# Kernel optimization log

Measured on AMD Instinct MI355X. Metric: run time of the kernel, lower is better.

Reference implementation:

```python
import jax, jax.numpy as jnp
import numpy as np

B, N, F_IN, F_OUT = 8, 2048, 128, 64
ALPHA = 0.2  # LeakyReLU negative slope
NEG_INF = -9e15


def setup_inputs() -> dict:
    key = jax.random.key(0)
    k1, k2, k3, k4 = jax.random.split(key, 4)
    h = jax.random.normal(k1, (B, N, F_IN), dtype=jnp.float32)
    adj = jax.random.randint(k2, (B, N, N), 0, 2, dtype=jnp.int32)
    # xavier_uniform with gain=1.414 approximated by scaled normals (values are arbitrary params)
    W = jax.random.normal(k3, (F_IN, F_OUT), dtype=jnp.float32) * (1.414 * np.sqrt(2.0 / (F_IN + F_OUT)))
    a = jax.random.normal(k4, (2 * F_OUT, 1), dtype=jnp.float32) * (1.414 * np.sqrt(2.0 / (2 * F_OUT + 1)))
    return {"h": h, "adj": adj, "W": W, "a": a}


def reference(h, adj, W, a):
    # Wh: [B, N, F_out]
    Wh = jnp.einsum('bnf,fo->bno', h, W)
    Fo = W.shape[1]
    a1 = a[:Fo, 0]   # [F_out]
    a2 = a[Fo:, 0]   # [F_out]
    # e[b,i,j] = leakyrelu(Wh[b,i]@a1 + Wh[b,j]@a2)  (== cat(Wh_i,Wh_j)@a, same math, no N^2*2F blowup)
    e1 = jnp.einsum('bno,o->bn', Wh, a1)  # [B, N]
    e2 = jnp.einsum('bno,o->bn', Wh, a2)  # [B, N]
    e = e1[:, :, None] + e2[:, None, :]   # [B, N, N]
    e = jnp.where(e > 0, e, ALPHA * e)    # LeakyReLU
    e = jnp.where(adj > 0, e, NEG_INF)    # mask non-edges
    attention = jax.nn.softmax(e, axis=-1)
    # dropout is identity in inference mode (deterministic reference)
    h_prime = jnp.einsum('bij,bjo->bio', attention, Wh)  # [B, N, F_out]
    return jax.nn.elu(h_prime)  # concat=True branch
```

## Files before the change

kernel.cpp:

```cpp
#include <hip/hip_runtime.h>
#include <hip/hip_bf16.h>

#define BB 8
#define NN 2048
#define FIN 128
#define FO 64
#define ALPHA 0.2f
#define SPLITS 4

typedef __attribute__((ext_vector_type(8))) short bf16x8;
typedef __attribute__((ext_vector_type(4))) float f32x4;
typedef __attribute__((ext_vector_type(4))) int i32x4;

__device__ inline short f2bf(float x) {
    unsigned u = __float_as_uint(x);
    u += 0x7fffu + ((u >> 16) & 1u);
    return (short)(u >> 16);
}

__global__ __launch_bounds__(256) void wh_kernel(
    const float* __restrict__ h, const float* __restrict__ W,
    const float* __restrict__ a, float* __restrict__ e1, float* __restrict__ e2,
    __hip_bfloat16* __restrict__ whT)
{
    __shared__ float hs[32][FIN];
    const int r0 = blockIdx.x * 32;
    const int t = threadIdx.x;
    const float4* hsrc = (const float4*)(h + (size_t)r0 * FIN);
    float4* hdst = (float4*)(&hs[0][0]);
#pragma unroll
    for (int k = 0; k < 4; k++) hdst[t + 256 * k] = hsrc[t + 256 * k];
    __syncthreads();

    const int o = t & 63;
    const int wv = t >> 6;
    float acc[8];
#pragma unroll
    for (int rr = 0; rr < 8; rr++) acc[rr] = 0.f;

    for (int f = 0; f < FIN; f += 4) {
        const float w0 = W[(f + 0) * FO + o];
        const float w1 = W[(f + 1) * FO + o];
        const float w2 = W[(f + 2) * FO + o];
        const float w3 = W[(f + 3) * FO + o];
#pragma unroll
        for (int rr = 0; rr < 8; rr++) {
            float4 hv = *(const float4*)&hs[wv * 8 + rr][f];
            acc[rr] = fmaf(hv.x, w0, acc[rr]);
            acc[rr] = fmaf(hv.y, w1, acc[rr]);
            acc[rr] = fmaf(hv.z, w2, acc[rr]);
            acc[rr] = fmaf(hv.w, w3, acc[rr]);
        }
    }

    const float a1 = a[o], a2 = a[FO + o];
    const int b = r0 / NN;
    const int ib0 = r0 - b * NN;
#pragma unroll
    for (int rr = 0; rr < 8; rr++) {
        const int ib = ib0 + wv * 8 + rr;
        const float w = acc[rr];
        whT[((size_t)(b * FO + o)) * NN + ib] = __float2bfloat16(w);
        float v1 = w * a1, v2 = w * a2;
#pragma unroll
        for (int m = 32; m >= 1; m >>= 1) {
            v1 += __shfl_xor(v1, m, 64);
            v2 += __shfl_xor(v2, m, 64);
        }
        if (o == 0) { e1[r0 + wv * 8 + rr] = v1; e2[r0 + wv * 8 + rr] = v2; }
    }
}

__global__ __launch_bounds__(256) void e2max_kernel(
    const float* __restrict__ e2, float* __restrict__ e2max)
{
    const int b = blockIdx.x;
    const int t = threadIdx.x;
    float m = -1e30f;
    for (int j = t; j < NN; j += 256) m = fmaxf(m, e2[b * NN + j]);
#pragma unroll
    for (int k = 32; k >= 1; k >>= 1) m = fmaxf(m, __shfl_xor(m, k, 64));
    __shared__ float red[4];
    if ((t & 63) == 0) red[t >> 6] = m;
    __syncthreads();
    if (t == 0) e2max[b] = fmaxf(fmaxf(red[0], red[1]), fmaxf(red[2], red[3]));
}

__global__ __launch_bounds__(256) void attn_kernel(
    const int* __restrict__ adj, const float* __restrict__ e1,
    const float* __restrict__ e2, const float* __restrict__ e2max,
    const __hip_bfloat16* __restrict__ whT,
    float* __restrict__ acc_ws,
    float* __restrict__ l_ws)
{
    const int t = threadIdx.x;
    const int wave = t >> 6, lane = t & 63;
    const int w = blockIdx.x * 4 + wave;
    const int s  = w & (SPLITS - 1);
    const int it = (w >> 2) & 127;
    const int b  = w >> 9;
    const int i0 = it * 16;
    const int m = lane & 15, q = lane >> 4;
    const int i = i0 + m;

    const float e1v = e1[b * NN + i];
    float mi = e1v + e2max[b];
    mi = mi > 0.f ? mi : ALPHA * mi;

    const int jbase = s * (NN / SPLITS);
    const int* adjrow = adj + ((size_t)(b * NN + i)) * NN;
    const float* e2b = e2 + b * NN;
    const short* wT = (const short*)(whT + (size_t)b * FO * NN);

    f32x4 acc0 = {0.f,0.f,0.f,0.f}, acc1 = acc0, acc2 = acc0, acc3 = acc0;
    float lsum = 0.f;

    for (int j0 = jbase; j0 < jbase + NN / SPLITS; j0 += 32) {
        const int jq = j0 + q * 8;
        i32x4 ad0 = *(const i32x4*)(adjrow + jq);
        i32x4 ad1 = *(const i32x4*)(adjrow + jq + 4);
        f32x4 ev0 = *(const f32x4*)(e2b + jq);
        f32x4 ev1 = *(const f32x4*)(e2b + jq + 4);

        bf16x8 af;
#pragma unroll
        for (int jj = 0; jj < 8; jj++) {
            const int   av = (jj < 4) ? ad0[jj] : ad1[jj - 4];
            const float e2j = (jj < 4) ? ev0[jj] : ev1[jj - 4];
            float e = e1v + e2j;
            e = e > 0.f ? e : ALPHA * e;
            const float pe = (av > 0) ? __expf(e - mi) : 0.f;
            lsum += pe;
            af[jj] = f2bf(pe);
        }

        bf16x8 b0 = *(const bf16x8*)(wT + (size_t)( 0 + m) * NN + jq);
        bf16x8 b1 = *(const bf16x8*)(wT + (size_t)(16 + m) * NN + jq);
        bf16x8 b2 = *(const bf16x8*)(wT + (size_t)(32 + m) * NN + jq);
        bf16x8 b3 = *(const bf16x8*)(wT + (size_t)(48 + m) * NN + jq);

        acc0 = __builtin_amdgcn_mfma_f32_16x16x32_bf16(af, b0, acc0, 0, 0, 0);
        acc1 = __builtin_amdgcn_mfma_f32_16x16x32_bf16(af, b1, acc1, 0, 0, 0);
        acc2 = __builtin_amdgcn_mfma_f32_16x16x32_bf16(af, b2, acc2, 0, 0, 0);
        acc3 = __builtin_amdgcn_mfma_f32_16x16x32_bf16(af, b3, acc3, 0, 0, 0);
    }

    lsum += __shfl_xor(lsum, 16, 64);
    lsum += __shfl_xor(lsum, 32, 64);
    if (q == 0) l_ws[(size_t)s * BB * NN + b * NN + i] = lsum;

    float* aout = acc_ws + ((size_t)s * BB * NN + b * NN) * FO;
#pragma unroll
    for (int ot = 0; ot < 4; ot++) {
        f32x4 av = (ot == 0) ? acc0 : (ot == 1) ? acc1 : (ot == 2) ? acc2 : acc3;
#pragma unroll
        for (int reg = 0; reg < 4; reg++) {
            const int row = i0 + q * 4 + reg;
            aout[(size_t)row * FO + ot * 16 + m] = av[reg];
        }
    }
}

__global__ __launch_bounds__(256) void final_kernel(
    const float* __restrict__ acc_ws, const float* __restrict__ l_ws,
    float* __restrict__ out)
{
    const int gid = blockIdx.x * 256 + threadIdx.x;
    const int r = gid >> 6, o = gid & 63;
    float sum = 0.f;
#pragma unroll
    for (int s = 0; s < SPLITS; s++) sum += acc_ws[((size_t)s * BB * NN + r) * FO + o];
    float l = 0.f;
#pragma unroll
    for (int s = 0; s < SPLITS; s++) l += l_ws[(size_t)s * BB * NN + r];
    l = fmaxf(l, 1e-38f);
    const float v = sum / l;
    out[gid] = v > 0.f ? v : (__expf(v) - 1.f);
}

extern "C" void kernel_launch(void* const* d_in, const int* in_sizes, int n_in,
                              void* d_out, int out_size, void* d_ws, size_t ws_size,
                              hipStream_t stream) {
    const float* h   = (const float*)d_in[0];
    const int*   adj = (const int*)d_in[1];
    const float* W   = (const float*)d_in[2];
    const float* a   = (const float*)d_in[3];
    float* out = (float*)d_out;

    char* ws = (char*)d_ws;
    __hip_bfloat16* whT = (__hip_bfloat16*)ws;
    size_t off = (size_t)BB * FO * NN * sizeof(__hip_bfloat16);
    float* e1 = (float*)(ws + off);  off += (size_t)BB * NN * 4;
    float* e2 = (float*)(ws + off);  off += (size_t)BB * NN * 4;
    float* e2m = (float*)(ws + off); off += 256;
    float* acc_ws = (float*)(ws + off); off += (size_t)SPLITS * BB * NN * FO * 4;
    float* l_ws = (float*)(ws + off);

    wh_kernel<<<(BB * NN) / 32, 256, 0, stream>>>(h, W, a, e1, e2, whT);
    e2max_kernel<<<BB, 256, 0, stream>>>(e2, e2m);
    attn_kernel<<<(BB * (NN / 16) * SPLITS) / 4, 256, 0, stream>>>(adj, e1, e2, e2m, whT, acc_ws, l_ws);
    final_kernel<<<(BB * NN * FO) / 256, 256, 0, stream>>>(acc_ws, l_ws, out);
}
```

Baseline: 247.0 us.

## Fuse split-K reduction into attention kernel with LDS-staged adjacency and MFMA-packed Wh

Each block now handles 16 rows over the full j range, with its 4 waves splitting j and combining partial accumulators and row sums in LDS. This removes the global split workspace and the separate final kernel. Adjacency tiles are staged into LDS with global_load_lds so the global reads are coalesced across full rows. Wh is stored pre-swizzled in MFMA B-fragment order so each lane does one contiguous 16-byte load. The trade-offs are a barrier per 256-column chunk with no double buffering, and a grid of 1024 blocks instead of 4096 waves spread across blocks.

New measurement: 217.2 us. -12.0%, faster.

```diff
diff --git a/kernel.cpp b/kernel.cpp
--- a/kernel.cpp
+++ b/kernel.cpp
@@ -6,11 +6,17 @@
 #define FIN 128
 #define FO 64
 #define ALPHA 0.2f
-#define SPLITS 4
 
 typedef __attribute__((ext_vector_type(8))) short bf16x8;
 typedef __attribute__((ext_vector_type(4))) float f32x4;
 typedef __attribute__((ext_vector_type(4))) int i32x4;
+
+typedef __attribute__((address_space(1))) const void gvoid;
+typedef __attribute__((address_space(3))) void lvoid;
+
+__device__ inline void gl_lds16(const void* g, void* l) {
+    __builtin_amdgcn_global_load_lds((gvoid*)g, (lvoid*)l, 16, 0, 0);
+}
 
 __device__ inline short f2bf(float x) {
     unsigned u = __float_as_uint(x);
@@ -21,7 +27,7 @@
 __global__ __launch_bounds__(256) void wh_kernel(
     const float* __restrict__ h, const float* __restrict__ W,
     const float* __restrict__ a, float* __restrict__ e1, float* __restrict__ e2,
-    __hip_bfloat16* __restrict__ whT)
+    short* __restrict__ whF)
 {
     __shared__ float hs[32][FIN];
     const int r0 = blockIdx.x * 32;
@@ -53,19 +59,26 @@
         }
     }
 
+    const int b   = r0 / NN;
+    const int ib0 = r0 - b * NN;
+    const int ibb = ib0 + wv * 8;
+    const int jc  = ibb >> 5;
+    const int qq  = (ibb >> 3) & 3;
+    const int ot  = o >> 4, mm = o & 15;
+    const int L   = mm + qq * 16;
+    bf16x8 frag;
+#pragma unroll
+    for (int rr = 0; rr < 8; rr++) frag[rr] = f2bf(acc[rr]);
+    *(bf16x8*)(whF + ((((size_t)(b * 64 + jc) * 4 + ot) * 64 + L) * 8)) = frag;
+
     const float a1 = a[o], a2 = a[FO + o];
-    const int b = r0 / NN;
-    const int ib0 = r0 - b * NN;
 #pragma unroll
     for (int rr = 0; rr < 8; rr++) {
-        const int ib = ib0 + wv * 8 + rr;
-        const float w = acc[rr];
-        whT[((size_t)(b * FO + o)) * NN + ib] = __float2bfloat16(w);
-        float v1 = w * a1, v2 = w * a2;
-#pragma unroll
-        for (int m = 32; m >= 1; m >>= 1) {
-            v1 += __shfl_xor(v1, m, 64);
-            v2 += __shfl_xor(v2, m, 64);
+        float v1 = acc[rr] * a1, v2 = acc[rr] * a2;
+#pragma unroll
+        for (int msk = 32; msk >= 1; msk >>= 1) {
+            v1 += __shfl_xor(v1, msk, 64);
+            v2 += __shfl_xor(v2, msk, 64);
         }
         if (o == 0) { e1[r0 + wv * 8 + rr] = v1; e2[r0 + wv * 8 + rr] = v2; }
     }
@@ -86,96 +99,106 @@
     if (t == 0) e2max[b] = fmaxf(fmaxf(red[0], red[1]), fmaxf(red[2], red[3]));
 }
 
+struct SMemS { int adj[16][260]; float e2[256]; };
+struct SMemC { float comb[4][16][64]; float lsum[4][16]; };
+union SMemU { SMemS s; SMemC c; };
+
 __global__ __launch_bounds__(256) void attn_kernel(
     const int* __restrict__ adj, const float* __restrict__ e1,
     const float* __restrict__ e2, const float* __restrict__ e2max,
-    const __hip_bfloat16* __restrict__ whT,
-    float* __restrict__ acc_ws,
-    float* __restrict__ l_ws)
+    const short* __restrict__ whF, float* __restrict__ out)
 {
-    const int t = threadIdx.x;
-    const int wave = t >> 6, lane = t & 63;
-    const int w = blockIdx.x * 4 + wave;
-    const int s  = w & (SPLITS - 1);
-    const int it = (w >> 2) & 127;
-    const int b  = w >> 9;
-    const int i0 = it * 16;
+    __shared__ SMemU sm;
+    const int t = threadIdx.x, w = t >> 6, lane = t & 63;
     const int m = lane & 15, q = lane >> 4;
-    const int i = i0 + m;
+    const int blk = blockIdx.x;
+    const int b  = blk >> 7;
+    const int i0 = (blk & 127) * 16;
+    const int i  = i0 + m;
 
     const float e1v = e1[b * NN + i];
     float mi = e1v + e2max[b];
     mi = mi > 0.f ? mi : ALPHA * mi;
 
-    const int jbase = s * (NN / SPLITS);
-    const int* adjrow = adj + ((size_t)(b * NN + i)) * NN;
-    const float* e2b = e2 + b * NN;
-    const short* wT = (const short*)(whT + (size_t)b * FO * NN);
+    const short* whFb = whF + (size_t)b * (64 * 4 * 64 * 8);
+    const int* arow0 = adj + ((size_t)(b * NN + i0)) * NN + lane * 4;
+    const float* e2g = e2 + b * NN + lane * 4;
 
     f32x4 acc0 = {0.f,0.f,0.f,0.f}, acc1 = acc0, acc2 = acc0, acc3 = acc0;
     float lsum = 0.f;
 
-    for (int j0 = jbase; j0 < jbase + NN / SPLITS; j0 += 32) {
-        const int jq = j0 + q * 8;
-        i32x4 ad0 = *(const i32x4*)(adjrow + jq);
-        i32x4 ad1 = *(const i32x4*)(adjrow + jq + 4);
-        f32x4 ev0 = *(const f32x4*)(e2b + jq);
-        f32x4 ev1 = *(const f32x4*)(e2b + jq + 4);
-
-        bf16x8 af;
-#pragma unroll
-        for (int jj = 0; jj < 8; jj++) {
-            const int   av = (jj < 4) ? ad0[jj] : ad1[jj - 4];
-            const float e2j = (jj < 4) ? ev0[jj] : ev1[jj - 4];
-            float e = e1v + e2j;
-            e = e > 0.f ? e : ALPHA * e;
-            const float pe = (av > 0) ? __expf(e - mi) : 0.f;
-            lsum += pe;
-            af[jj] = f2bf(pe);
-        }
-
-        bf16x8 b0 = *(const bf16x8*)(wT + (size_t)( 0 + m) * NN + jq);
-        bf16x8 b1 = *(const bf16x8*)(wT + (size_t)(16 + m) * NN + jq);
-        bf16x8 b2 = *(const bf16x8*)(wT + (size_t)(32 + m) * NN + jq);
-        bf16x8 b3 = *(const bf16x8*)(wT + (size_t)(48 + m) * NN + jq);
-
-        acc0 = __builtin_amdgcn_mfma_f32_16x16x32_bf16(af, b0, acc0, 0, 0, 0);
-        acc1 = __builtin_amdgcn_mfma_f32_16x16x32_bf16(af, b1, acc1, 0, 0, 0);
-        acc2 = __builtin_amdgcn_mfma_f32_16x16x32_bf16(af, b2, acc2, 0, 0, 0);
-        acc3 = __builtin_amdgcn_mfma_f32_16x16x32_bf16(af, b3, acc3, 0, 0, 0);
+    for (int j0 = 0; j0 < NN; j0 += 256) {
+#pragma unroll
+        for (int k = 0; k < 4; k++) {
+            const int r = w * 4 + k;
+            gl_lds16(arow0 + (size_t)r * NN + j0, &sm.s.adj[r][0]);
+        }
+        if (w == 0) gl_lds16(e2g + j0, &sm.s.e2[0]);
+        __syncthreads();
+
+#pragma unroll
+        for (int s2 = 0; s2 < 2; s2++) {
+            const int col = w * 64 + s2 * 32 + q * 8;
+            i32x4 a0 = *(const i32x4*)&sm.s.adj[m][col];
+            i32x4 a1 = *(const i32x4*)&sm.s.adj[m][col + 4];
+            f32x4 ev0 = *(const f32x4*)&sm.s.e2[col];
+            f32x4 ev1 = *(const f32x4*)&sm.s.e2[col + 4];
+
+            bf16x8 af;
+#pragma unroll
+            for (int jj = 0; jj < 8; jj++) {
+                const int   av  = (jj < 4) ? a0[jj]      : a1[jj - 4];
+                const float e2j = (jj < 4) ? ev0[jj]     : ev1[jj - 4];
+                float e = e1v + e2j;
+                e = e > 0.f ? e : ALPHA * e;
+                const float pe = (av > 0) ? __expf(e - mi) : 0.f;
+                lsum += pe;
+                af[jj] = f2bf(pe);
+            }
+
+            const int jc = (j0 + w * 64 + s2 * 32) >> 5;
+            const short* bfp = whFb + (size_t)jc * 2048 + lane * 8;
+            bf16x8 b0 = *(const bf16x8*)(bfp);
+            bf16x8 b1 = *(const bf16x8*)(bfp + 512);
+            bf16x8 b2 = *(const bf16x8*)(bfp + 1024);
+            bf16x8 b3 = *(const bf16x8*)(bfp + 1536);
+
+            acc0 = __builtin_amdgcn_mfma_f32_16x16x32_bf16(af, b0, acc0, 0, 0, 0);
+            acc1 = __builtin_amdgcn_mfma_f32_16x16x32_bf16(af, b1, acc1, 0, 0, 0);
+            acc2 = __builtin_amdgcn_mfma_f32_16x16x32_bf16(af, b2, acc2, 0, 0, 0);
+            acc3 = __builtin_amdgcn_mfma_f32_16x16x32_bf16(af, b3, acc3, 0, 0, 0);
+        }
+        __syncthreads();
     }
 
     lsum += __shfl_xor(lsum, 16, 64);
     lsum += __shfl_xor(lsum, 32, 64);
-    if (q == 0) l_ws[(size_t)s * BB * NN + b * NN + i] = lsum;
-
-    float* aout = acc_ws + ((size_t)s * BB * NN + b * NN) * FO;
+    if (q == 0) sm.c.lsum[w][m] = lsum;
 #pragma unroll
     for (int ot = 0; ot < 4; ot++) {
         f32x4 av = (ot == 0) ? acc0 : (ot == 1) ? acc1 : (ot == 2) ? acc2 : acc3;
 #pragma unroll
-        for (int reg = 0; reg < 4; reg++) {
-            const int row = i0 + q * 4 + reg;
-            aout[(size_t)row * FO + ot * 16 + m] = av[reg];
-        }
-    }
-}
-
-__global__ __launch_bounds__(256) void final_kernel(
-    const float* __restrict__ acc_ws, const float* __restrict__ l_ws,
-    float* __restrict__ out)
-{
-    const int gid = blockIdx.x * 256 + threadIdx.x;
-    const int r = gid >> 6, o = gid & 63;
-    float sum = 0.f;
-#pragma unroll
-    for (int s = 0; s < SPLITS; s++) sum += acc_ws[((size_t)s * BB * NN + r) * FO + o];
-    float l = 0.f;
-#pragma unroll
-    for (int s = 0; s < SPLITS; s++) l += l_ws[(size_t)s * BB * NN + r];
-    l = fmaxf(l, 1e-38f);
-    const float v = sum / l;
-    out[gid] = v > 0.f ? v : (__expf(v) - 1.f);
+        for (int reg = 0; reg < 4; reg++)
+            sm.c.comb[w][q * 4 + reg][ot * 16 + m] = av[reg];
+    }
+    __syncthreads();
+
+    const int row = t >> 4, c0 = (t & 15) * 4;
+    f32x4 sum = *(const f32x4*)&sm.c.comb[0][row][c0];
+#pragma unroll
+    for (int ww = 1; ww < 4; ww++) {
+        f32x4 sv = *(const f32x4*)&sm.c.comb[ww][row][c0];
+        sum.x += sv.x; sum.y += sv.y; sum.z += sv.z; sum.w += sv.w;
+    }
+    float l = sm.c.lsum[0][row] + sm.c.lsum[1][row] + sm.c.lsum[2][row] + sm.c.lsum[3][row];
+    l = fmaxf(l, 1e-30f);
+    const float rl = 1.f / l;
+    float vr[4] = { sum.x * rl, sum.y * rl, sum.z * rl, sum.w * rl };
+    f32x4 res;
+#pragma unroll
+    for (int kk = 0; kk < 4; kk++)
+        res[kk] = vr[kk] > 0.f ? vr[kk] : (__expf(vr[kk]) - 1.f);
+    *(f32x4*)&out[((size_t)(b * NN + i0 + row)) * FO + c0] = res;
 }
 
 extern "C" void kernel_launch(void* const* d_in, const int* in_sizes, int n_in,
@@ -188,16 +211,13 @@
     float* out = (float*)d_out;
 
     char* ws = (char*)d_ws;
-    __hip_bfloat16* whT = (__hip_bfloat16*)ws;
-    size_t off = (size_t)BB * FO * NN * sizeof(__hip_bfloat16);
-    float* e1 = (float*)(ws + off);  off += (size_t)BB * NN * 4;
-    float* e2 = (float*)(ws + off);  off += (size_t)BB * NN * 4;
-    float* e2m = (float*)(ws + off); off += 256;
-    float* acc_ws = (float*)(ws + off); off += (size_t)SPLITS * BB * NN * FO * 4;
-    float* l_ws = (float*)(ws + off);
-
-    wh_kernel<<<(BB * NN) / 32, 256, 0, stream>>>(h, W, a, e1, e2, whT);
+    short* whF = (short*)ws;
+    size_t off = (size_t)BB * 64 * 4 * 64 * 8 * sizeof(short);
+    float* e1  = (float*)(ws + off);  off += (size_t)BB * NN * 4;
+    float* e2  = (float*)(ws + off);  off += (size_t)BB * NN * 4;
+    float* e2m = (float*)(ws + off);
+
+    wh_kernel<<<(BB * NN) / 32, 256, 0, stream>>>(h, W, a, e1, e2, whF);
     e2max_kernel<<<BB, 256, 0, stream>>>(e2, e2m);
-    attn_kernel<<<(BB * (NN / 16) * SPLITS) / 4, 256, 0, stream>>>(adj, e1, e2, e2m, whT, acc_ws, l_ws);
-    final_kernel<<<(BB * NN * FO) / 256, 256, 0, stream>>>(acc_ws, l_ws, out);
-}
+    attn_kernel<<<BB * (NN / 16), 256, 0, stream>>>(adj, e1, e2, e2m, whF, out);
+}
```
